# Optimization experiments

Hardware: AMD Instinct MI355X
Metric: run time of the kernel (lower is better)

The kernel has to match this reference:

```python
import jax, jax.numpy as jnp
import numpy as np

B, N, T, D = 2, 4, 512, 1024
DK, H, E = 64, 8, 6
D_ATTN = 512
DV = D_ATTN // H            # 64
DKP = 2 * DK                # PoPE doubles key dim -> 128
HE = H * E                  # 48
R = max(DK // 4, 1)         # LoRA rank 16
DA = int(DK * 1.618)        # 103
CC = D_ATTN                 # concat dim 512
DPG = max(int(CC * 0.618), 1)  # 316
ND = N * D
ROUTE_TEMP = 1.0


def _sinkhorn(M, n_iters=6):
    M = jnp.exp(M)
    for _ in range(n_iters):
        M = M / jnp.sum(M, -1, keepdims=True)
        M = M / jnp.sum(M, -2, keepdims=True)
    return M


def _pope(x, phi):
    mu = jax.nn.softplus(x)
    return jnp.concatenate([mu * jnp.cos(phi), mu * jnp.sin(phi)], -1)


def setup_inputs():
    ks = iter(jax.random.split(jax.random.key(0), 24))
    def rn(s, sc=0.01):
        return jax.random.normal(next(ks), s, jnp.float32) * sc
    return {
        'stream': jax.random.normal(next(ks), (B, N, T, D), jnp.float32),
        'freqs': 10000.0 ** (jnp.arange(DK, dtype=jnp.float32) / DK),
        'pope_delta_raw': jnp.zeros((DK,), jnp.float32),
        'W_q_w': rn((H, DK, D)), 'W_k_w': rn((H, DK, D)), 'W_v_w': rn((H, DV, D)),
        'q_router_w': rn((H, E, D), 0.02), 'kv_router_w': rn((H, E, D), 0.02),
        'lora_A_q': rn((HE, D, R)), 'lora_B_q': jnp.zeros((HE, R, DK), jnp.float32),
        'lora_A_k': rn((HE, D, R)), 'lora_B_k': jnp.zeros((HE, R, DK), jnp.float32),
        'lora_A_v': rn((HE, D, R)), 'lora_B_v': jnp.zeros((HE, R, DV), jnp.float32),
        'alpha_up_w': rn((HE, D, DA)), 'alpha_down_w': rn((HE, DA, DKP)),
        'beta_up_w': rn((HE, D, DA)), 'beta_down_w': rn((HE, DA, 1)),
        'mhc_norm_w': jnp.ones((HE, ND), jnp.float32),
        'phi_pre_w': rn((HE, N, ND)), 'phi_post_w': rn((HE, N, ND)),
        'phi_res_w': rn((HE, N * N, ND)),
        'b_pre': jnp.zeros((HE, N), jnp.float32), 'b_post': jnp.zeros((HE, N), jnp.float32),
        'b_res': jnp.zeros((HE, N, N), jnp.float32),
        'alpha_pre': jnp.ones((HE,), jnp.float32), 'alpha_post': jnp.ones((HE,), jnp.float32),
        'alpha_res': jnp.ones((HE,), jnp.float32),
        'batched_norm_w': jnp.ones((HE, D), jnp.float32),
        'W_pre_w': rn((HE, D, CC)), 'W_o_w': rn((D, CC)),
        'W_pg1_w': rn((HE, D, DPG)), 'W_pg2_w': rn((HE, DPG, D)),
    }


def reference(stream, freqs, pope_delta_raw, W_q_w, W_k_w, W_v_w, q_router_w, kv_router_w,
              lora_A_q, lora_B_q, lora_A_k, lora_B_k, lora_A_v, lora_B_v,
              alpha_up_w, alpha_down_w, beta_up_w, beta_down_w,
              mhc_norm_w, phi_pre_w, phi_post_w, phi_res_w, b_pre, b_post, b_res,
              alpha_pre, alpha_post, alpha_res, batched_norm_w,
              W_pre_w, W_o_w, W_pg1_w, W_pg2_w):
    positions = jnp.arange(T, dtype=jnp.float32)
    # ---- per-head top-1 routing (eval-mode argmax, straight-through probs) ----
    route_in = jnp.mean(stream, axis=1)                                # (B,T,D)
    q_logits = jnp.clip(jnp.einsum('btd,hed->hbte', route_in, q_router_w), -10, 10)
    kv_logits = jnp.clip(jnp.einsum('btd,hed->hbte', route_in, kv_router_w), -10, 10)
    q_probs = jax.nn.softmax(q_logits / ROUTE_TEMP, -1)
    kv_probs = jax.nn.softmax(kv_logits / ROUTE_TEMP, -1)
    q_oh = jax.nn.one_hot(jnp.argmax(q_logits, -1), E, dtype=stream.dtype)
    kv_oh = jax.nn.one_hot(jnp.argmax(kv_logits, -1), E, dtype=stream.dtype)
    eff_q = q_probs + jax.lax.stop_gradient(q_oh - q_probs)            # (H,B,T,E)
    eff_kv = kv_probs + jax.lax.stop_gradient(kv_oh - kv_probs)
    eff_q = eff_q.transpose(0, 3, 1, 2).reshape(HE, B, T)              # h-major, k=h*E+e
    eff_kv = eff_kv.transpose(0, 3, 1, 2).reshape(HE, B, T)
    # ---- batched MHC over all HE experts (dense form of active-set gather) ----
    x = stream.transpose(0, 2, 1, 3).reshape(B, T, ND)
    x = x * jax.lax.rsqrt(jnp.mean(jnp.square(x), -1, keepdims=True) + 1e-8)
    H_pre = jax.nn.sigmoid(alpha_pre[:, None, None, None] *
                           jnp.einsum('btd,knd->kbtn', x, phi_pre_w * mhc_norm_w[:, None, :])
                           + b_pre[:, None, None, :])
    H_post = 2 * jax.nn.sigmoid(alpha_post[:, None, None, None] *
                                jnp.einsum('btd,knd->kbtn', x, phi_post_w * mhc_norm_w[:, None, :])
                                + b_post[:, None, None, :])
    res = jnp.einsum('btd,knd->kbtn', x, phi_res_w * mhc_norm_w[:, None, :]).reshape(HE, B, T, N, N)
    H_res = _sinkhorn(alpha_res[:, None, None, None, None] * res + b_res[:, None, None, :, :])
    h_e = jnp.einsum('kbtn,bntd->kbtd', H_pre, stream)                 # (HE,B,T,D)
    h_e = h_e * jax.lax.rsqrt(jnp.mean(jnp.square(h_e), -1, keepdims=True) + 1e-8) * batched_norm_w[:, None, None, :]
    # ---- expert q/k/v with LoRA + PoPE ----
    phi = positions[:, None] * freqs[None, :]                          # (T,DK)
    phi_k = phi - 2 * jnp.pi * jax.nn.sigmoid(pope_delta_raw)[None, :]
    Wq = jnp.repeat(W_q_w, E, 0); Wk = jnp.repeat(W_k_w, E, 0); Wv = jnp.repeat(W_v_w, E, 0)
    def lora(h, A, Bm):
        return jnp.einsum('kbtr,kro->kbto', jax.nn.silu(jnp.einsum('kbtd,kdr->kbtr', h, A)), Bm)
    def l2n(v):
        return v * jax.lax.rsqrt(jnp.sum(jnp.square(v), -1, keepdims=True) + 1e-12)
    q_p = l2n(jnp.einsum('kbtd,kod->kbto', h_e, Wq) + lora(h_e, lora_A_q, lora_B_q))
    k_p = l2n(jnp.einsum('kbtd,kod->kbto', h_e, Wk) + lora(h_e, lora_A_k, lora_B_k))
    v_p = jnp.einsum('kbtd,kod->kbto', h_e, Wv) + lora(h_e, lora_A_v, lora_B_v)
    qmask = (jnp.arange(HE) % E > 0).astype(stream.dtype)[:, None, None, None]  # expert 0 = no-op for Q
    q_out = _pope(q_p, phi[None, None]) * qmask                        # (HE,B,T,DKP)
    k_out = _pope(k_p, phi_k[None, None])
    a_out = jax.nn.sigmoid(jnp.einsum('kbta,kap->kbtp', jax.nn.silu(jnp.einsum('kbtd,kda->kbta', h_e, alpha_up_w)), alpha_down_w))
    b_out = jax.nn.sigmoid(jnp.einsum('kbta,kap->kbtp', jax.nn.silu(jnp.einsum('kbtd,kda->kbta', h_e, beta_up_w)), beta_down_w))
    def mix(w, vals):
        return (w[..., None] * vals).reshape(H, E, B, T, vals.shape[-1]).sum(1)  # (H,B,T,*)
    q_buf = mix(eff_q, q_out); k_buf = mix(eff_kv, k_out); v_buf = mix(eff_kv, v_p)
    a_buf = mix(eff_kv, a_out); b_buf = mix(eff_kv, b_out)
    # ---- KDA delta-rule state recursion via lax.scan over time ----
    def step(S, xs):
        q_t, k_t, v_t, a_t, b_t = xs                                   # (H,B,dim)
        aS = a_t[..., None] * S                                        # (H,B,DKP,DV)
        ktaS = jnp.einsum('hbd,hbde->hbe', k_t, aS)
        S = aS + b_t[..., None] * (k_t[..., None] * (v_t - ktaS)[..., None, :])
        return S, jnp.einsum('hbd,hbde->hbe', q_t, S)
    tf = lambda z: jnp.moveaxis(z, 2, 0)                               # (T,H,B,*)
    S0 = jnp.zeros((H, B, DKP, DV), stream.dtype)
    _, outs = jax.lax.scan(step, S0, (tf(q_buf), tf(k_buf), tf(v_buf), tf(a_buf), tf(b_buf)))
    attn = outs.transpose(2, 0, 1, 3).reshape(B, T, H * DV)            # concat heads
    # ---- gates, output projection, MHC write-back ----
    pre_gate = jax.nn.sigmoid(jnp.einsum('kbt,kbtd,kdc->btc', eff_kv, h_e, W_pre_w))
    pg = jax.nn.silu(jnp.einsum('kbtd,kdp->kbtp', h_e, W_pg1_w))
    post_gate = jax.nn.sigmoid(jnp.einsum('kbt,kbtp,kpd->btd', eff_kv, pg, W_pg2_w))
    y = jnp.einsum('btc,dc->btd', attn * pre_gate, W_o_w) * post_gate
    Hres_acc = jnp.einsum('kbt,kbtnm->btnm', eff_kv, H_res) / H
    Hpost_acc = jnp.einsum('kbt,kbtn->btn', eff_kv, H_post) / H
    return jnp.einsum('btnm,bmtd->bntd', Hres_acc, stream) + jnp.einsum('btn,btd->bntd', Hpost_acc, y)
```

## Files before the change

### kernel.cpp

```cpp
#include <hip/hip_runtime.h>
#include <math.h>

#define DEV static __device__ __forceinline__

#define B_   2
#define N_   4
#define T_   512
#define D_   1024
#define DK_  64
#define H_   8
#define E_   6
#define DV_  64
#define DKP_ 128
#define HE_  48
#define R_   16
#define DA_  103
#define CC_  512
#define DPG_ 316
#define ND_  4096
#define U_   1024

typedef unsigned short u16;
typedef __attribute__((ext_vector_type(8))) unsigned short us8;
typedef __attribute__((ext_vector_type(8))) short bhalf8;
typedef __attribute__((ext_vector_type(4))) float f32x4;

struct P {
  const float *stream, *freqs, *pope_delta;
  const float *W_q, *W_k, *W_v, *q_rw, *kv_rw;
  const float *lA_q, *lB_q, *lA_k, *lB_k, *lA_v, *lB_v;
  const float *a_up, *a_dn, *b_up, *b_dn;
  const float *mhc_norm, *phi_pre, *phi_post, *phi_res;
  const float *b_pre, *b_post, *b_res, *al_pre, *al_post, *al_res;
  const float *bn_w, *W_pre, *W_o, *W_pg1, *W_pg2;
  int *qsel, *kvsel, *qcnt, *kvcnt, *qlist, *kvlist;
  float *scale, *mhc_partial;
  float *Hpre_q, *Hpre_kv, *Hres, *Hpost;
  float *kv_lin, *aup, *bup, *pre_logit, *post_logit;
  float *la_k, *la_v, *la_q, *q_lin;
  float *a_buf, *b_buf, *q_buf, *k_buf, *v_buf;
  float *attn, *y;
  float *out;
  u16 *he_kvB, *he_qB, *pgB;
  u16 *Bt0, *Bt1, *Bt2, *Bt3, *Bt4;
  float *phiT, *he_kvF, *he_qF, *pgF;
  float *WqT, *WkT, *WvT, *WoT;
};

DEV float sigm(float x){ return 1.f/(1.f+expf(-x)); }
DEV float softplus_(float x){ return x>0.f ? x+log1pf(expf(-x)) : log1pf(expf(x)); }
DEV float silu_(float x){ return x*sigm(x); }
DEV u16 f2b(float x){ unsigned u = __float_as_uint(x); u += 0x7FFFu + ((u>>16)&1u); return (u16)(u>>16); }

DEV float block_reduce_sum(float v, float* sm){
  __syncthreads();
  int lane = threadIdx.x & 63, w = threadIdx.x >> 6;
  for (int off=32; off; off>>=1) v += __shfl_down(v, off, 64);
  if (lane==0) sm[w] = v;
  __syncthreads();
  if (threadIdx.x == 0){
    float s = 0; int nw = blockDim.x >> 6;
    for (int i=0;i<nw;i++) s += sm[i];
    sm[0] = s;
  }
  __syncthreads();
  return sm[0];
}


__global__ void k_prep0(P p){
  int j = blockIdx.x; int k = j/24, r = j%24;
  const float* src;
  if (r < 4)      src = p.phi_pre  + (size_t)(k*4+r)*ND_;
  else if (r < 8) src = p.phi_post + (size_t)(k*4+(r-4))*ND_;
  else            src = p.phi_res  + (size_t)(k*16+(r-8))*ND_;
  const float* mn = p.mhc_norm + (size_t)k*ND_;
  u16* d = p.Bt0 + (size_t)j*ND_;
  for (int i = threadIdx.x; i < ND_; i += 256) d[i] = f2b(src[i]*mn[i]);
}

__global__ void k_prep1d(P p){
  int r = blockIdx.x, g = blockIdx.y, h = g/E_;
  u16* drow = p.Bt1 + (size_t)g*1216*1024 + (size_t)(r<128 ? r : 1194 + (r-128))*1024;
  const float* srow = (r<64) ? (p.W_k + ((size_t)h*64 + r)*1024)
                   : (r<128) ? (p.W_v + ((size_t)h*64 + (r-64))*1024) : nullptr;
  for (int k2 = threadIdx.x; k2 < 1024; k2 += 256)
    drow[k2] = (r<128) ? f2b(srow[k2]) : (u16)0;
}

__global__ void k_prep2d(P p){
  int r = blockIdx.x, g = blockIdx.y, h = g/E_;
  u16* drow = p.Bt2 + (size_t)g*128*1024 + (size_t)r*1024;
  const float* srow = p.W_q + ((size_t)h*64 + r)*1024;
  for (int k2 = threadIdx.x; k2 < 1024; k2 += 256) drow[k2] = f2b(srow[k2]);
}

__global__ void k_prep4(P p){
  int r = blockIdx.x;
  u16* drow = p.Bt4 + (size_t)r*512;
  const float* srow = p.W_o + (size_t)r*512;
  for (int c = threadIdx.x; c < 512; c += 256) drow[c] = f2b(srow[c]);
}

__global__ void k_prept(const float* src, long sstride, int ld, int ncols,
                        u16* dst, long dstride, int dld, int K, int Ksrc){
  __shared__ float t[32][33];
  const float* S = src + (size_t)blockIdx.z*sstride;
  u16* Dp = dst + (size_t)blockIdx.z*dstride;
  int k0 = blockIdx.x*32, c0 = blockIdx.y*32;
  int tx = threadIdx.x & 31, ty = threadIdx.x >> 5;
  #pragma unroll
  for (int i=0;i<32;i+=8){
    int k = k0+ty+i, c = c0+tx;
    t[ty+i][tx] = (k < Ksrc && c < ncols) ? S[(size_t)k*ld + c] : 0.f;
  }
  __syncthreads();
  #pragma unroll
  for (int i=0;i<32;i+=8){
    int c = c0+ty+i, k = k0+tx;
    if (c < ncols && k < K) Dp[(size_t)c*dld + k] = f2b(t[tx][ty+i]);
  }
}


__global__ void k_route(P p){
  int u = blockIdx.x, b = u>>9, t = u&511;
  __shared__ float ri[D_];
  __shared__ float lg[2][HE_];
  int tid = threadIdx.x;
  for (int d = tid; d < D_; d += 256){
    float s = 0;
    #pragma unroll
    for (int n = 0; n < N_; n++) s += p.stream[(((size_t)(b*N_+n)*T_)+t)*D_ + d];
    ri[d] = s * 0.25f;
  }
  __syncthreads();
  int lane = tid & 63, wv = tid >> 6;
  for (int j = wv; j < 2*HE_; j += 4){
    const float* w = (j < HE_ ? p.q_rw : p.kv_rw) + (size_t)(j % HE_)*D_;
    float acc = 0;
    for (int d = lane; d < D_; d += 64) acc += ri[d]*w[d];
    for (int off=32; off; off>>=1) acc += __shfl_down(acc, off, 64);
    if (lane==0) lg[j/HE_][j%HE_] = acc;
  }
  __syncthreads();
  if (tid < 16){
    int h = tid & 7, which = tid >> 3;
    const float* L = lg[which] + h*E_;
    float best = fminf(fmaxf(L[0],-10.f),10.f); int bi=0;
    for (int e=1;e<E_;e++){ float v=fminf(fmaxf(L[e],-10.f),10.f); if (v>best){best=v;bi=e;} }
    int g = h*E_+bi;
    if (which==0){ p.qsel[h*U_+u]=bi;  int pos=atomicAdd(&p.qcnt[g],1);  p.qlist[g*U_+pos]=u; }
    else         { p.kvsel[h*U_+u]=bi; int pos=atomicAdd(&p.kvcnt[g],1); p.kvlist[g*U_+pos]=u; }
  }
}

__global__ void k_xscale(P p){
  int u = blockIdx.x, b = u>>9, t = u&511;
  __shared__ float sm[8];
  float ss = 0;
  for (int i = threadIdx.x; i < ND_; i += 256){
    int n = i >> 10, d = i & 1023;
    float v = p.stream[(((size_t)(b*N_+n)*T_)+t)*D_ + d];
    ss += v*v;
  }
  ss = block_reduce_sum(ss, sm);
  if (threadIdx.x==0) p.scale[u] = rsqrtf(ss/(float)ND_ + 1e-8f);
}


template<int MODE>
__global__ __launch_bounds__(256) void k_mgemm(P p){
  const int n0 = blockIdx.x * 128;
  const int m0 = blockIdx.y * 128;
  const int g  = blockIdx.z;
  const int h  = g / E_;
  int K, NO, cnt;
  const int* list = nullptr;
  const u16* Bsrc;
  if (MODE==0){ K=1024; NO=1152; cnt=U_; Bsrc=p.Bt0; }
  else if (MODE==1){ K=1024; NO=1194; cnt=p.kvcnt[g]; list=p.kvlist+g*U_; Bsrc=p.Bt1+(size_t)g*1216*1024; }
  else if (MODE==2){ K=1024; NO=80;   cnt=p.qcnt[g];  list=p.qlist +g*U_; Bsrc=p.Bt2+(size_t)g*128*1024; }
  else if (MODE==3){ K=320;  NO=1024; cnt=p.kvcnt[g]; list=p.kvlist+g*U_; Bsrc=p.Bt3+(size_t)g*1024*320; }
  else { K=512; NO=1024; cnt=U_; Bsrc=p.Bt4; }
  if (m0 >= cnt) return;
  const int rows = min(128, cnt - m0);

  __shared__ u16 Asl[128*32];
  __shared__ u16 Bsl[128*32];
  __shared__ int toks[128];
  const int tid = threadIdx.x;
  if (tid < 128){
    if (MODE==0||MODE==4) toks[tid] = m0 + tid;
    else toks[tid] = (tid < rows) ? list[m0+tid] : list[m0];
  }
  __syncthreads();

  f32x4 acc[4][4];
  #pragma unroll
  for (int i=0;i<4;i++)
    #pragma unroll
    for (int j=0;j<4;j++) acc[i][j] = (f32x4)(0.f);

  const int lane = tid & 63, wv = tid >> 6;
  const int wr = (wv>>1)*64, wc = (wv&1)*64;
  const int l16 = lane & 15, kce = lane >> 4;

  for (int k0 = 0; k0 < K; k0 += 32){
    #pragma unroll
    for (int pass=0; pass<2; pass++){
      int m = (tid>>2) + pass*64;
      int kc4 = tid & 3;
      int ks = k0 + kc4*8;
      us8 av;
      if (MODE==1){
        int u = toks[m];
        av = *(const us8*)&p.he_kvB[((size_t)(h*U_+u))*1024 + ks];
      } else if (MODE==2){
        int u = toks[m];
        av = *(const us8*)&p.he_qB[((size_t)(h*U_+u))*1024 + ks];
      } else if (MODE==3){
        int u = toks[m];
        av = *(const us8*)&p.pgB[((size_t)(h*U_+u))*320 + ks];
      } else if (MODE==0){
        int u = toks[m]; int bb=u>>9, tt=u&511;
        int fk = g*1024 + ks;
        int n = fk>>10, d = fk&1023;
        const float* sp = p.stream + (((size_t)(bb*N_+n)*T_)+tt)*D_ + d;
        float sc = p.scale[u];
        float4 x0 = *(const float4*)sp, x1 = *(const float4*)(sp+4);
        av[0]=f2b(x0.x*sc); av[1]=f2b(x0.y*sc); av[2]=f2b(x0.z*sc); av[3]=f2b(x0.w*sc);
        av[4]=f2b(x1.x*sc); av[5]=f2b(x1.y*sc); av[6]=f2b(x1.z*sc); av[7]=f2b(x1.w*sc);
      } else {
        int u = toks[m];
        const float* ap = p.attn + (size_t)u*CC_ + ks;
        const float* pp = p.pre_logit + (size_t)u*CC_ + ks;
        float4 a0 = *(const float4*)ap, a1 = *(const float4*)(ap+4);
        float4 q0 = *(const float4*)pp, q1 = *(const float4*)(pp+4);
        av[0]=f2b(a0.x*sigm(q0.x)); av[1]=f2b(a0.y*sigm(q0.y));
        av[2]=f2b(a0.z*sigm(q0.z)); av[3]=f2b(a0.w*sigm(q0.w));
        av[4]=f2b(a1.x*sigm(q1.x)); av[5]=f2b(a1.y*sigm(q1.y));
        av[6]=f2b(a1.z*sigm(q1.z)); av[7]=f2b(a1.w*sigm(q1.w));
      }
      *(us8*)&Asl[m*32 + kc4*8] = av;
    }
    #pragma unroll
    for (int pass=0; pass<2; pass++){
      int n = (tid>>2) + pass*64;
      int kc4 = tid & 3;
      int ks = k0 + kc4*8;
      int gn = n0 + n;
      us8 bv = (us8)((u16)0);
      if (MODE==1){ if (gn < 1216) bv = *(const us8*)&Bsrc[(size_t)gn*1024 + ks]; }
      else if (MODE==0){ bv = *(const us8*)&Bsrc[(size_t)gn*4096 + g*1024 + ks]; }
      else if (MODE==2){ bv = *(const us8*)&Bsrc[(size_t)gn*1024 + ks]; }
      else if (MODE==3){ bv = *(const us8*)&Bsrc[(size_t)gn*320 + ks]; }
      else { bv = *(const us8*)&Bsrc[(size_t)gn*512 + ks]; }
      *(us8*)&Bsl[n*32 + kc4*8] = bv;
    }
    __syncthreads();
    bhalf8 af[4], bf4[4];
    #pragma unroll
    for (int i=0;i<4;i++) af[i] = *(const bhalf8*)&Asl[(wr + i*16 + l16)*32 + kce*8];
    #pragma unroll
    for (int j=0;j<4;j++) bf4[j] = *(const bhalf8*)&Bsl[(wc + j*16 + l16)*32 + kce*8];
    #pragma unroll
    for (int i=0;i<4;i++)
      #pragma unroll
      for (int j=0;j<4;j++)
        acc[i][j] = __builtin_amdgcn_mfma_f32_16x16x32_bf16(af[i], bf4[j], acc[i][j], 0, 0, 0);
    __syncthreads();
  }

  #pragma unroll
  for (int i=0;i<4;i++){
    #pragma unroll
    for (int r=0;r<4;r++){
      int rl = wr + i*16 + kce*4 + r;
      if (rl >= rows) continue;
      int u = toks[rl];
      #pragma unroll
      for (int j=0;j<4;j++){
        int cg = n0 + wc + j*16 + l16;
        if (cg >= NO) continue;
        float v = acc[i][j][r];
        if (MODE==0){
          p.mhc_partial[(size_t)g*U_*1152 + (size_t)u*1152 + cg] = v;
        } else if (MODE==1){
          size_t base = (size_t)(h*U_+u);
          if (cg < 128)       p.kv_lin[base*128 + cg] = v;
          else if (cg < 231)  p.aup[base*DA_ + (cg-128)] = silu_(v);
          else if (cg < 334)  p.bup[base*DA_ + (cg-231)] = silu_(v);
          else if (cg < 846)  atomicAdd(&p.pre_logit[(size_t)u*CC_ + (cg-334)], v);
          else if (cg < 1162) p.pgB[base*320 + (cg-846)] = f2b(silu_(v));
          else if (cg < 1178) p.la_k[base*R_ + (cg-1162)] = silu_(v);
          else                p.la_v[base*R_ + (cg-1178)] = silu_(v);
        } else if (MODE==2){
          size_t base = (size_t)(h*U_+u);
          if (cg < 64) p.q_lin[base*64 + cg] = v;
          else         p.la_q[base*R_ + (cg-64)] = silu_(v);
        } else if (MODE==3){
          atomicAdd(&p.post_logit[(size_t)u*D_ + cg], v);
        } else {
          p.y[(size_t)u*D_ + cg] = v * sigm(p.post_logit[(size_t)u*D_ + cg]);
        }
      }
    }
  }
}

#define BM 128
#define BN 128
#define BKF 32

template<int MODE>
__global__ __launch_bounds__(256) void k_gemm_f32(P p){
  const int n0 = blockIdx.x * BN;
  const int m0 = blockIdx.y * BM;
  const int g  = blockIdx.z;
  const int h  = g / E_;
  int K, NO, cnt, kbase = 0;
  const int* list = nullptr;
  if (MODE==0){ K=1024; NO=1152; cnt=U_; kbase = g*1024; }
  else if (MODE==1){ K=D_;   NO=1194; cnt=p.kvcnt[g]; list=p.kvlist + g*U_; }
  else if (MODE==2){ K=D_;   NO=80;   cnt=p.qcnt[g];  list=p.qlist  + g*U_; }
  else if (MODE==3){ K=DPG_; NO=D_;   cnt=p.kvcnt[g]; list=p.kvlist + g*U_; }
  else { K=CC_; NO=D_; cnt=U_; }
  if (m0 >= cnt) return;
  const int rows = min(BM, cnt - m0);

  __shared__ __align__(16) float As[BKF][BM+4];
  __shared__ __align__(16) float Bs[BKF][BN+4];
  __shared__ int toks[BM];
  const int tid = threadIdx.x;
  for (int i = tid; i < BM; i += 256){
    if (MODE==1||MODE==2||MODE==3) toks[i] = (i < rows) ? list[m0+i] : 0;
    else toks[i] = m0 + i;
  }
  __syncthreads();

  float acc[8][8];
  #pragma unroll
  for (int i=0;i<8;i++)
    #pragma unroll
    for(int j=0;j<8;j++) acc[i][j]=0.f;
  const int wave = tid >> 6, lane = tid & 63;
  const int wr = wave >> 1, wc = wave & 1;
  const int lr = lane >> 3, lc = lane & 7;
  const int a0 = wr*64 + lr*8, b0 = wc*64 + lc*8;

  for (int k0 = 0; k0 < K; k0 += BKF){
    #pragma unroll
    for (int i=0;i<16;i++){
      int idx = tid + 256*i;
      int r = idx >> 5, kk = idx & 31;
      int kg = k0 + kk;
      float v = 0.f;
      if (r < rows && kg < K){
        int u = toks[r];
        if (MODE==0){
          int kgg = kbase + kg;
          int b=u>>9, t=u&511, n=kgg>>10, d=kgg&1023;
          v = p.stream[(((size_t)(b*N_+n)*T_)+t)*D_ + d] * p.scale[u];
        } else if (MODE==1) v = p.he_kvF[((size_t)(h*U_+u))*D_ + kg];
        else if (MODE==2)   v = p.he_qF [((size_t)(h*U_+u))*D_ + kg];
        else if (MODE==3)   v = p.pgF  [((size_t)(h*U_+u))*DPG_ + kg];
        else {
          size_t o = (size_t)u*CC_ + kg;
          v = p.attn[o] * sigm(p.pre_logit[o]);
        }
      }
      As[kk][r] = v;
    }
    #pragma unroll
    for (int i=0;i<16;i++){
      int idx = tid + 256*i;
      int kk = idx >> 7, c = idx & 127;
      int kg = k0 + kk, cg = n0 + c;
      float v = 0.f;
      if (kg < K && cg < NO){
        if (MODE==0) v = p.phiT[(size_t)(kbase+kg)*1152 + cg];
        else if (MODE==1){
          const float* ptr; int ld, loc;
          if (cg < 64){        ptr = p.WkT   + (size_t)h*D_*64;   ld=64;   loc=cg; }
          else if (cg < 128){  ptr = p.WvT   + (size_t)h*D_*64;   ld=64;   loc=cg-64; }
          else if (cg < 231){  ptr = p.a_up  + (size_t)g*D_*DA_;  ld=DA_;  loc=cg-128; }
          else if (cg < 334){  ptr = p.b_up  + (size_t)g*D_*DA_;  ld=DA_;  loc=cg-231; }
          else if (cg < 846){  ptr = p.W_pre + (size_t)g*D_*CC_;  ld=CC_;  loc=cg-334; }
          else if (cg < 1162){ ptr = p.W_pg1 + (size_t)g*D_*DPG_; ld=DPG_; loc=cg-846; }
          else if (cg < 1178){ ptr = p.lA_k  + (size_t)g*D_*R_;   ld=R_;   loc=cg-1162; }
          else {               ptr = p.lA_v  + (size_t)g*D_*R_;   ld=R_;   loc=cg-1178; }
          v = ptr[(size_t)kg*ld + loc];
        }
        else if (MODE==2){
          if (cg < 64) v = p.WqT[(size_t)h*D_*64 + (size_t)kg*64 + cg];
          else v = p.lA_q[(size_t)g*D_*R_ + (size_t)kg*R_ + (cg-64)];
        }
        else if (MODE==3) v = p.W_pg2[(size_t)g*DPG_*D_ + (size_t)kg*D_ + cg];
        else v = p.WoT[(size_t)kg*D_ + cg];
      }
      Bs[kk][c] = v;
    }
    __syncthreads();
    #pragma unroll 8
    for (int kk=0; kk<BKF; kk++){
      float a[8], b[8];
      *(float4*)&a[0] = *(const float4*)&As[kk][a0];
      *(float4*)&a[4] = *(const float4*)&As[kk][a0+4];
      *(float4*)&b[0] = *(const float4*)&Bs[kk][b0];
      *(float4*)&b[4] = *(const float4*)&Bs[kk][b0+4];
      #pragma unroll
      for (int i=0;i<8;i++)
        #pragma unroll
        for (int j=0;j<8;j++) acc[i][j] += a[i]*b[j];
    }
    __syncthreads();
  }

  #pragma unroll
  for (int i=0;i<8;i++){
    int rl = a0 + i;
    if (rl >= rows) continue;
    int u = toks[rl];
    #pragma unroll
    for (int j=0;j<8;j++){
      int cg = n0 + b0 + j;
      if (cg >= NO) continue;
      float v = acc[i][j];
      if (MODE==0){
        p.mhc_partial[(size_t)g*U_*1152 + (size_t)u*1152 + cg] = v;
      } else if (MODE==1){
        size_t base = (size_t)(h*U_+u);
        if (cg < 128)       p.kv_lin[base*128 + cg] = v;
        else if (cg < 231)  p.aup[base*DA_ + (cg-128)] = silu_(v);
        else if (cg < 334)  p.bup[base*DA_ + (cg-231)] = silu_(v);
        else if (cg < 846)  atomicAdd(&p.pre_logit[(size_t)u*CC_ + (cg-334)], v);
        else if (cg < 1162) p.pgF[base*DPG_ + (cg-846)] = silu_(v);
        else if (cg < 1178) p.la_k[base*R_ + (cg-1162)] = silu_(v);
        else                p.la_v[base*R_ + (cg-1178)] = silu_(v);
      } else if (MODE==2){
        size_t base = (size_t)(h*U_+u);
        if (cg < 64) p.q_lin[base*64 + cg] = v;
        else         p.la_q[base*R_ + (cg-64)] = silu_(v);
      } else if (MODE==3){
        atomicAdd(&p.post_logit[(size_t)u*D_ + cg], v);
      } else {
        p.y[(size_t)u*D_ + cg] = v * sigm(p.post_logit[(size_t)u*D_ + cg]);
      }
    }
  }
}

__global__ void k_tr(const float* src, float* dst, int R, int C){
  __shared__ float t[32][33];
  int m = blockIdx.z;
  const float* S = src + (size_t)m*R*C;
  float* Dp = dst + (size_t)m*R*C;
  int c0 = blockIdx.x*32, r0 = blockIdx.y*32;
  int tx = threadIdx.x & 31, ty = threadIdx.x >> 5;
  #pragma unroll
  for (int i=0;i<32;i+=8)
    t[ty+i][tx] = S[(size_t)(r0+ty+i)*C + c0+tx];
  __syncthreads();
  #pragma unroll
  for (int i=0;i<32;i+=8)
    Dp[(size_t)(c0+ty+i)*R + r0+tx] = t[tx][ty+i];
}

__global__ void k_phiT(P p){
  __shared__ float t[64][65];
  int jt = blockIdx.x % 18, dt = blockIdx.x / 18;
  int tx = threadIdx.x & 63, ty = threadIdx.x >> 6;
  #pragma unroll
  for (int i=0;i<64;i+=4){
    int j = jt*64 + ty + i;
    int k = j/24, r = j%24;
    const float* src;
    if (r < 4)      src = p.phi_pre  + (size_t)(k*4+r)*ND_;
    else if (r < 8) src = p.phi_post + (size_t)(k*4+(r-4))*ND_;
    else            src = p.phi_res  + (size_t)(k*16+(r-8))*ND_;
    int d = dt*64 + tx;
    t[ty+i][tx] = src[d] * p.mhc_norm[(size_t)k*ND_ + d];
  }
  __syncthreads();
  #pragma unroll
  for (int i=0;i<64;i+=4){
    int d = dt*64 + ty + i;
    p.phiT[(size_t)d*1152 + jt*64 + tx] = t[tx][ty+i];
  }
}


DEV float lgread(const float* Pp, int j){
  const size_t S = (size_t)U_*1152;
  return Pp[j] + Pp[j+S] + Pp[j+2*S] + Pp[j+3*S];
}

__global__ void k_mhcsel(P p){
  int u = blockIdx.x;
  int tid = threadIdx.x;
  __shared__ float racc[8][16];
  __shared__ float pacc[8][4];
  if (tid < 8){
    int h = tid;
    const float* lg = p.mhc_partial + (size_t)u*1152;
    int kq = h*E_ + p.qsel[h*U_+u];
    for (int n=0;n<4;n++)
      p.Hpre_q[(size_t)(h*U_+u)*4 + n] = sigm(p.al_pre[kq]*lgread(lg,kq*24+n) + p.b_pre[kq*4+n]);
    int kk = h*E_ + p.kvsel[h*U_+u];
    for (int n=0;n<4;n++)
      p.Hpre_kv[(size_t)(h*U_+u)*4 + n] = sigm(p.al_pre[kk]*lgread(lg,kk*24+n) + p.b_pre[kk*4+n]);
    for (int n=0;n<4;n++)
      pacc[h][n] = 2.f*sigm(p.al_post[kk]*lgread(lg,kk*24+4+n) + p.b_post[kk*4+n]);
    float M[4][4];
    for (int n=0;n<4;n++)
      for (int m=0;m<4;m++)
        M[n][m] = expf(p.al_res[kk]*lgread(lg,kk*24+8+n*4+m) + p.b_res[kk*16+n*4+m]);
    for (int it=0; it<6; it++){
      for (int n=0;n<4;n++){ float s=M[n][0]+M[n][1]+M[n][2]+M[n][3]; float r=1.f/s;
        for(int m=0;m<4;m++) M[n][m]*=r; }
      for (int m=0;m<4;m++){ float s=M[0][m]+M[1][m]+M[2][m]+M[3][m]; float r=1.f/s;
        for(int n=0;n<4;n++) M[n][m]*=r; }
    }
    for (int n=0;n<4;n++) for (int m=0;m<4;m++) racc[h][n*4+m] = M[n][m];
  }
  __syncthreads();
  if (tid < 16){
    float s=0; for (int h=0;h<8;h++) s += racc[h][tid];
    p.Hres[(size_t)u*16 + tid] = s * 0.125f;
  }
  if (tid < 4){
    float s=0; for (int h=0;h<8;h++) s += pacc[h][tid];
    p.Hpost[(size_t)u*4 + tid] = s * 0.125f;
  }
}

template<int BF>
__global__ void k_he(P p){
  int id = blockIdx.x;
  int path = id >> 13;
  int h = (id >> 10) & 7;
  int u = id & 1023;
  int b = u>>9, t = u&511;
  int sel = path ? p.kvsel[h*U_+u] : p.qsel[h*U_+u];
  int k = h*E_ + sel;
  const float* Hp = (path ? p.Hpre_kv : p.Hpre_q) + (size_t)(h*U_+u)*4;
  float w0=Hp[0], w1=Hp[1], w2=Hp[2], w3=Hp[3];
  float v[4];
  float ss = 0;
  int tid = threadIdx.x;
  #pragma unroll
  for (int j=0;j<4;j++){
    int d = tid + j*256;
    float s0 = p.stream[(((size_t)(b*N_+0)*T_)+t)*D_ + d];
    float s1 = p.stream[(((size_t)(b*N_+1)*T_)+t)*D_ + d];
    float s2 = p.stream[(((size_t)(b*N_+2)*T_)+t)*D_ + d];
    float s3 = p.stream[(((size_t)(b*N_+3)*T_)+t)*D_ + d];
    v[j] = w0*s0 + w1*s1 + w2*s2 + w3*s3;
    ss += v[j]*v[j];
  }
  __shared__ float sm[8];
  ss = block_reduce_sum(ss, sm);
  float sc = rsqrtf(ss/(float)D_ + 1e-8f);
  #pragma unroll
  for (int j=0;j<4;j++){
    int d = tid + j*256;
    float o = v[j]*sc*p.bn_w[(size_t)k*D_ + d];
    if (BF){
      u16* out = (path ? p.he_kvB : p.he_qB) + (size_t)(h*U_+u)*D_;
      out[d] = f2b(o);
    } else {
      float* out = (path ? p.he_kvF : p.he_qF) + (size_t)(h*U_+u)*D_;
      out[d] = o;
    }
  }
}

__global__ void k_stage2(P p){
  int id = blockIdx.x;
  int h = id >> 10, u = id & 1023;
  int t = u & 511;
  int k = h*E_ + p.kvsel[h*U_+u];
  size_t base = (size_t)(h*U_+u);
  __shared__ float s_au[DA_], s_bu[DA_], s_lk[R_], s_lv[R_], s_kl[64], s_vl[64];
  int tid = threadIdx.x;
  if (tid < DA_){ s_au[tid] = p.aup[base*DA_+tid]; s_bu[tid] = p.bup[base*DA_+tid]; }
  if (tid < R_){ s_lk[tid] = p.la_k[base*R_+tid]; s_lv[tid] = p.la_v[base*R_+tid]; }
  if (tid >= 64 && tid < 128){
    s_kl[tid-64] = p.kv_lin[base*128 + (tid-64)];
    s_vl[tid-64] = p.kv_lin[base*128 + 64 + (tid-64)];
  }
  __syncthreads();
  {
    float acc = 0;
    const float* W = p.a_dn + (size_t)k*DA_*DKP_;
    for (int a=0;a<DA_;a++) acc += s_au[a]*W[a*DKP_ + tid];
    p.a_buf[base*DKP_ + tid] = sigm(acc);
  }
  if (tid == 0){
    float acc = 0;
    const float* W = p.b_dn + (size_t)k*DA_;
    for (int a=0;a<DA_;a++) acc += s_bu[a]*W[a];
    p.b_buf[base] = sigm(acc);
  }
  if (tid < 64){
    int o = tid;
    float lbk=0.f, lbv=0.f;
    for (int r=0;r<R_;r++){
      lbk += s_lk[r]*p.lB_k[((size_t)k*R_+r)*DK_ + o];
      lbv += s_lv[r]*p.lB_v[((size_t)k*R_+r)*DV_ + o];
    }
    float kl = s_kl[o] + lbk;
    float ss = kl*kl;
    for (int off=1; off<64; off<<=1) ss += __shfl_xor(ss, off, 64);
    float kp = kl * rsqrtf(ss + 1e-12f);
    float mu = softplus_(kp);
    float ph = (float)t * p.freqs[o] - 6.2831855f * sigm(p.pope_delta[o]);
    p.k_buf[base*DKP_ + o]      = mu * cosf(ph);
    p.k_buf[base*DKP_ + 64 + o] = mu * sinf(ph);
    p.v_buf[base*DV_ + o] = s_vl[o] + lbv;
  }
}

__global__ void k_stage2q(P p){
  int id = blockIdx.x;
  int h = id >> 10, u = id & 1023;
  int t = u & 511;
  int sel = p.qsel[h*U_+u];
  size_t base = (size_t)(h*U_+u);
  int o = threadIdx.x;
  if (sel == 0){
    p.q_buf[base*DKP_ + o] = 0.f;
    p.q_buf[base*DKP_ + 64 + o] = 0.f;
    return;
  }
  int k = h*E_ + sel;
  float lbq = 0.f;
  for (int r=0;r<R_;r++) lbq += p.la_q[base*R_+r]*p.lB_q[((size_t)k*R_+r)*DK_+o];
  float ql = p.q_lin[base*64 + o] + lbq;
  float ss = ql*ql;
  for (int off=1; off<64; off<<=1) ss += __shfl_xor(ss, off, 64);
  float qp = ql*rsqrtf(ss + 1e-12f);
  float mu = softplus_(qp);
  float ph = (float)t * p.freqs[o];
  p.q_buf[base*DKP_ + o]      = mu*cosf(ph);
  p.q_buf[base*DKP_ + 64 + o] = mu*sinf(ph);
}

__global__ __launch_bounds__(512) void k_scan(P p){
  int h = blockIdx.x >> 1, b = blockIdx.x & 1;
  int tid = threadIdx.x;
  int e = tid & 63, d8 = tid >> 6;
  float S[16];
  #pragma unroll
  for (int i=0;i<16;i++) S[i]=0.f;
  __shared__ float sq[128], sk[128], sa[128], sv[64];
  __shared__ float sb[1];
  __shared__ float part[8][64];
  __shared__ float part2[8][64];
  float r0=0.f, r1=0.f;
  {
    size_t base = (size_t)(h*U_ + b*T_);
    if (tid < 128){ r0 = p.q_buf[base*128+tid]; r1 = p.k_buf[base*128+tid]; }
    else if (tid < 256){ r0 = p.a_buf[base*128 + (tid-128)]; }
    else if (tid < 320){ r0 = p.v_buf[base*64 + (tid-256)]; }
    else if (tid == 320){ r0 = p.b_buf[base]; }
  }
  for (int t=0;t<T_;t++){
    if (tid < 128){ sq[tid]=r0; sk[tid]=r1; }
    else if (tid < 256){ sa[tid-128]=r0; }
    else if (tid < 320){ sv[tid-256]=r0; }
    else if (tid == 320){ sb[0]=r0; }
    __syncthreads();
    if (t+1 < T_){
      size_t base = (size_t)(h*U_ + b*T_ + t+1);
      if (tid < 128){ r0 = p.q_buf[base*128+tid]; r1 = p.k_buf[base*128+tid]; }
      else if (tid < 256){ r0 = p.a_buf[base*128 + (tid-128)]; }
      else if (tid < 320){ r0 = p.v_buf[base*64 + (tid-256)]; }
      else if (tid == 320){ r0 = p.b_buf[base]; }
    }
    int db = d8*16;
    float pa = 0.f;
    #pragma unroll
    for (int i=0;i<16;i++) pa += sk[db+i]*sa[db+i]*S[i];
    part[d8][e] = pa;
    __syncthreads();
    float w = sv[e];
    #pragma unroll
    for (int j=0;j<8;j++) w -= part[j][e];
    float bs = sb[0];
    float o = 0.f;
    #pragma unroll
    for (int i=0;i<16;i++){
      S[i] = sa[db+i]*S[i] + bs*sk[db+i]*w;
      o += sq[db+i]*S[i];
    }
    part2[d8][e] = o;
    __syncthreads();
    if (tid < 64){
      float s=0;
      #pragma unroll
      for (int j=0;j<8;j++) s += part2[j][tid];
      p.attn[(size_t)(b*T_+t)*CC_ + h*64 + tid] = s;
    }
  }
}

__global__ void k_final(P p){
  int u = blockIdx.x, b=u>>9, t=u&511;
  __shared__ float hr[16], hp[4];
  if (threadIdx.x < 16) hr[threadIdx.x] = p.Hres[(size_t)u*16+threadIdx.x];
  if (threadIdx.x < 4)  hp[threadIdx.x] = p.Hpost[(size_t)u*4+threadIdx.x];
  __syncthreads();
  for (int d = threadIdx.x; d < D_; d += 256){
    float yv = p.y[(size_t)u*D_ + d];
    float sm0 = p.stream[(((size_t)(b*N_+0)*T_)+t)*D_ + d];
    float sm1 = p.stream[(((size_t)(b*N_+1)*T_)+t)*D_ + d];
    float sm2 = p.stream[(((size_t)(b*N_+2)*T_)+t)*D_ + d];
    float sm3 = p.stream[(((size_t)(b*N_+3)*T_)+t)*D_ + d];
    #pragma unroll
    for (int n=0;n<4;n++){
      float v = hr[n*4+0]*sm0 + hr[n*4+1]*sm1 + hr[n*4+2]*sm2 + hr[n*4+3]*sm3 + hp[n]*yv;
      p.out[(((size_t)(b*N_+n)*T_)+t)*D_ + d] = v;
    }
  }
}


extern "C" void kernel_launch(void* const* d_in, const int* in_sizes, int n_in,
                              void* d_out, int out_size, void* d_ws, size_t ws_size,
                              hipStream_t stream){
  P p;
  p.stream = (const float*)d_in[0];
  p.freqs = (const float*)d_in[1];
  p.pope_delta = (const float*)d_in[2];
  p.W_q = (const float*)d_in[3]; p.W_k = (const float*)d_in[4]; p.W_v = (const float*)d_in[5];
  p.q_rw = (const float*)d_in[6]; p.kv_rw = (const float*)d_in[7];
  p.lA_q = (const float*)d_in[8];  p.lB_q = (const float*)d_in[9];
  p.lA_k = (const float*)d_in[10]; p.lB_k = (const float*)d_in[11];
  p.lA_v = (const float*)d_in[12]; p.lB_v = (const float*)d_in[13];
  p.a_up = (const float*)d_in[14]; p.a_dn = (const float*)d_in[15];
  p.b_up = (const float*)d_in[16]; p.b_dn = (const float*)d_in[17];
  p.mhc_norm = (const float*)d_in[18];
  p.phi_pre = (const float*)d_in[19]; p.phi_post = (const float*)d_in[20]; p.phi_res = (const float*)d_in[21];
  p.b_pre = (const float*)d_in[22]; p.b_post = (const float*)d_in[23]; p.b_res = (const float*)d_in[24];
  p.al_pre = (const float*)d_in[25]; p.al_post = (const float*)d_in[26]; p.al_res = (const float*)d_in[27];
  p.bn_w = (const float*)d_in[28];
  p.W_pre = (const float*)d_in[29]; p.W_o = (const float*)d_in[30];
  p.W_pg1 = (const float*)d_in[31]; p.W_pg2 = (const float*)d_in[32];
  p.out = (float*)d_out;

  char* w = (char*)d_ws;
  size_t off = 0;
  auto alloc = [&](size_t bytes)->void*{
    void* r = w + off;
    off = (off + bytes + 255) & ~(size_t)255;
    return r;
  };
  p.qsel   = (int*)alloc(H_*U_*4);
  p.kvsel  = (int*)alloc(H_*U_*4);
  p.qcnt   = (int*)alloc(HE_*4);
  p.kvcnt  = (int*)alloc(HE_*4);
  p.qlist  = (int*)alloc((size_t)HE_*U_*4);
  p.kvlist = (int*)alloc((size_t)HE_*U_*4);
  p.scale  = (float*)alloc(U_*4);
  p.mhc_partial = (float*)alloc((size_t)4*U_*1152*4);
  p.Hpre_q  = (float*)alloc((size_t)H_*U_*4*4);
  p.Hpre_kv = (float*)alloc((size_t)H_*U_*4*4);
  p.Hres    = (float*)alloc((size_t)U_*16*4);
  p.Hpost   = (float*)alloc((size_t)U_*4*4);
  p.kv_lin  = (float*)alloc((size_t)H_*U_*128*4);
  p.aup     = (float*)alloc((size_t)H_*U_*DA_*4);
  p.bup     = (float*)alloc((size_t)H_*U_*DA_*4);
  p.pre_logit  = (float*)alloc((size_t)U_*CC_*4);
  p.post_logit = (float*)alloc((size_t)U_*D_*4);
  p.la_k    = (float*)alloc((size_t)H_*U_*R_*4);
  p.la_v    = (float*)alloc((size_t)H_*U_*R_*4);
  p.la_q    = (float*)alloc((size_t)H_*U_*R_*4);
  p.q_lin   = (float*)alloc((size_t)H_*U_*64*4);
  p.a_buf   = (float*)alloc((size_t)H_*U_*DKP_*4);
  p.b_buf   = (float*)alloc((size_t)H_*U_*4);
  p.q_buf   = (float*)alloc((size_t)H_*U_*DKP_*4);
  p.k_buf   = (float*)alloc((size_t)H_*U_*DKP_*4);
  p.v_buf   = (float*)alloc((size_t)H_*U_*DV_*4);
  p.attn    = (float*)alloc((size_t)U_*CC_*4);
  p.y       = (float*)alloc((size_t)U_*D_*4);
  size_t common_off = off;

  p.he_kvB = (u16*)alloc((size_t)H_*U_*D_*2);
  p.he_qB  = (u16*)alloc((size_t)H_*U_*D_*2);
  p.pgB    = (u16*)alloc((size_t)H_*U_*320*2);
  p.Bt0    = (u16*)alloc((size_t)1152*4096*2);
  p.Bt1    = (u16*)alloc((size_t)HE_*1216*1024*2);
  p.Bt2    = (u16*)alloc((size_t)HE_*128*1024*2);
  p.Bt3    = (u16*)alloc((size_t)HE_*1024*320*2);
  p.Bt4    = (u16*)alloc((size_t)1024*512*2);
  bool mfma = (off <= ws_size);

  if (!mfma){
    off = common_off;
    p.phiT   = (float*)alloc((size_t)ND_*1152*4);
    p.he_kvF = (float*)alloc((size_t)H_*U_*D_*4);
    p.he_qF  = (float*)alloc((size_t)H_*U_*D_*4);
    p.pgF    = (float*)alloc((size_t)H_*U_*DPG_*4);
    p.WqT    = (float*)alloc((size_t)H_*D_*64*4);
    p.WkT    = (float*)alloc((size_t)H_*D_*64*4);
    p.WvT    = (float*)alloc((size_t)H_*D_*64*4);
    p.WoT    = (float*)alloc((size_t)CC_*D_*4);
    if (off > ws_size) return;
  }

  hipMemsetAsync(p.qcnt, 0, HE_*4, stream);
  hipMemsetAsync(p.kvcnt, 0, HE_*4, stream);
  hipMemsetAsync(p.pre_logit, 0, (size_t)U_*CC_*4, stream);
  hipMemsetAsync(p.post_logit, 0, (size_t)U_*D_*4, stream);

  if (mfma){
    hipMemsetAsync(p.pgB, 0, (size_t)H_*U_*320*2, stream);
    hipMemsetAsync(p.Bt2, 0, (size_t)HE_*128*1024*2, stream);
    k_prep0<<<1152,256,0,stream>>>(p);
    k_prep1d<<<dim3(150,48),256,0,stream>>>(p);
    size_t b1s = (size_t)1216*1024;
    k_prept<<<dim3(32, 4,48),256,0,stream>>>(p.a_up,  (long)1024*DA_, DA_, DA_, p.Bt1+ 128*1024, b1s, 1024, 1024, 1024);
    k_prept<<<dim3(32, 4,48),256,0,stream>>>(p.b_up,  (long)1024*DA_, DA_, DA_, p.Bt1+ 231*1024, b1s, 1024, 1024, 1024);
    k_prept<<<dim3(32,16,48),256,0,stream>>>(p.W_pre, (long)1024*CC_, CC_, CC_, p.Bt1+ 334*1024, b1s, 1024, 1024, 1024);
    k_prept<<<dim3(32,10,48),256,0,stream>>>(p.W_pg1, (long)1024*DPG_,DPG_,DPG_,p.Bt1+ 846*1024, b1s, 1024, 1024, 1024);
    k_prept<<<dim3(32, 1,48),256,0,stream>>>(p.lA_k,  (long)1024*R_,  R_,  R_,  p.Bt1+1162*1024, b1s, 1024, 1024, 1024);
    k_prept<<<dim3(32, 1,48),256,0,stream>>>(p.lA_v,  (long)1024*R_,  R_,  R_,  p.Bt1+1178*1024, b1s, 1024, 1024, 1024);
    k_prep2d<<<dim3(64,48),256,0,stream>>>(p);
    k_prept<<<dim3(32, 1,48),256,0,stream>>>(p.lA_q,  (long)1024*R_,  R_,  R_,  p.Bt2+  64*1024, (long)128*1024, 1024, 1024, 1024);
    k_prept<<<dim3(10,32,48),256,0,stream>>>(p.W_pg2, (long)DPG_*1024,1024,1024,p.Bt3,           (long)1024*320,  320,  320,  316);
    k_prep4<<<1024,256,0,stream>>>(p);

    k_route<<<U_,256,0,stream>>>(p);
    k_xscale<<<U_,256,0,stream>>>(p);
    k_mgemm<0><<<dim3(9,8,4),256,0,stream>>>(p);
    k_mhcsel<<<U_,64,0,stream>>>(p);
    k_he<1><<<2*H_*U_,256,0,stream>>>(p);
    k_mgemm<1><<<dim3(10,8,48),256,0,stream>>>(p);
    k_mgemm<2><<<dim3(1,8,48),256,0,stream>>>(p);
    k_stage2<<<H_*U_,128,0,stream>>>(p);
    k_stage2q<<<H_*U_,64,0,stream>>>(p);
    k_mgemm<3><<<dim3(8,8,48),256,0,stream>>>(p);
    k_scan<<<16,512,0,stream>>>(p);
    k_mgemm<4><<<dim3(8,8,1),256,0,stream>>>(p);
    k_final<<<U_,256,0,stream>>>(p);
  } else {
    k_tr<<<dim3(32,2,8),256,0,stream>>>(p.W_q, p.WqT, 64, 1024);
    k_tr<<<dim3(32,2,8),256,0,stream>>>(p.W_k, p.WkT, 64, 1024);
    k_tr<<<dim3(32,2,8),256,0,stream>>>(p.W_v, p.WvT, 64, 1024);
    k_tr<<<dim3(16,32,1),256,0,stream>>>(p.W_o, p.WoT, 1024, 512);
    k_phiT<<<1152,256,0,stream>>>(p);
    k_route<<<U_,256,0,stream>>>(p);
    k_xscale<<<U_,256,0,stream>>>(p);
    k_gemm_f32<0><<<dim3(9,8,4),256,0,stream>>>(p);
    k_mhcsel<<<U_,64,0,stream>>>(p);
    k_he<0><<<2*H_*U_,256,0,stream>>>(p);
    k_gemm_f32<1><<<dim3(10,8,48),256,0,stream>>>(p);
    k_gemm_f32<2><<<dim3(1,8,48),256,0,stream>>>(p);
    k_stage2<<<H_*U_,128,0,stream>>>(p);
    k_stage2q<<<H_*U_,64,0,stream>>>(p);
    k_gemm_f32<3><<<dim3(8,8,48),256,0,stream>>>(p);
    k_scan<<<16,512,0,stream>>>(p);
    k_gemm_f32<4><<<dim3(8,8,1),256,0,stream>>>(p);
    k_final<<<U_,256,0,stream>>>(p);
  }
}
```

Baseline: 1.537 ms.

## Fuse xscale into routing, merge stage2q into stage2, restructure scan, drop fp32 fallback

The RMS scale computation moves into the routing kernel, which also writes a pre-scaled bf16 copy of the stream. The first MFMA GEMM then loads bf16 directly instead of converting fp32 on the fly. The q-side stage2 work is folded into the kv stage2 kernel, so one launch replaces two. The sequential scan is rewritten with 256 threads holding 32 state elements each, reading k/a from global memory into registers and double-buffering q in shared memory, which cuts barriers per step. The unused fp32 fallback path is removed, and the fallback no longer exists if the workspace is too small.

```diff
diff --git a/kernel.cpp b/kernel.cpp
--- a/kernel.cpp
+++ b/kernel.cpp
@@ -41,10 +41,9 @@
   float *a_buf, *b_buf, *q_buf, *k_buf, *v_buf;
   float *attn, *y;
   float *out;
+  u16 *xb;
   u16 *he_kvB, *he_qB, *pgB;
   u16 *Bt0, *Bt1, *Bt2, *Bt3, *Bt4;
-  float *phiT, *he_kvF, *he_qF, *pgF;
-  float *WqT, *WkT, *WvT, *WoT;
 };
 
 DEV float sigm(float x){ return 1.f/(1.f+expf(-x)); }
@@ -127,14 +126,30 @@
   int u = blockIdx.x, b = u>>9, t = u&511;
   __shared__ float ri[D_];
   __shared__ float lg[2][HE_];
+  __shared__ float sm[8];
   int tid = threadIdx.x;
-  for (int d = tid; d < D_; d += 256){
-    float s = 0;
-    #pragma unroll
-    for (int n = 0; n < N_; n++) s += p.stream[(((size_t)(b*N_+n)*T_)+t)*D_ + d];
-    ri[d] = s * 0.25f;
-  }
-  __syncthreads();
+  float sv[4][4]; float ss = 0.f;
+  #pragma unroll
+  for (int j=0;j<4;j++){
+    int d = tid + j*256;
+    float acc = 0;
+    #pragma unroll
+    for (int n = 0; n < 4; n++){
+      float v = p.stream[(((size_t)(b*N_+n)*T_)+t)*D_ + d];
+      sv[j][n] = v; acc += v; ss += v*v;
+    }
+    ri[d] = acc * 0.25f;
+  }
+  ss = block_reduce_sum(ss, sm);
+  float sc = rsqrtf(ss/(float)ND_ + 1e-8f);
+  if (tid==0) p.scale[u] = sc;
+  #pragma unroll
+  for (int j=0;j<4;j++){
+    int d = tid + j*256;
+    #pragma unroll
+    for (int n=0;n<4;n++)
+      p.xb[(size_t)u*ND_ + n*D_ + d] = f2b(sv[j][n]*sc);
+  }
   int lane = tid & 63, wv = tid >> 6;
   for (int j = wv; j < 2*HE_; j += 4){
     const float* w = (j < HE_ ? p.q_rw : p.kv_rw) + (size_t)(j % HE_)*D_;
@@ -153,19 +168,6 @@
     if (which==0){ p.qsel[h*U_+u]=bi;  int pos=atomicAdd(&p.qcnt[g],1);  p.qlist[g*U_+pos]=u; }
     else         { p.kvsel[h*U_+u]=bi; int pos=atomicAdd(&p.kvcnt[g],1); p.kvlist[g*U_+pos]=u; }
   }
-}
-
-__global__ void k_xscale(P p){
-  int u = blockIdx.x, b = u>>9, t = u&511;
-  __shared__ float sm[8];
-  float ss = 0;
-  for (int i = threadIdx.x; i < ND_; i += 256){
-    int n = i >> 10, d = i & 1023;
-    float v = p.stream[(((size_t)(b*N_+n)*T_)+t)*D_ + d];
-    ss += v*v;
-  }
-  ss = block_reduce_sum(ss, sm);
-  if (threadIdx.x==0) p.scale[u] = rsqrtf(ss/(float)ND_ + 1e-8f);
 }
 
 
@@ -223,14 +225,8 @@
         int u = toks[m];
         av = *(const us8*)&p.pgB[((size_t)(h*U_+u))*320 + ks];
       } else if (MODE==0){
-        int u = toks[m]; int bb=u>>9, tt=u&511;
-        int fk = g*1024 + ks;
-        int n = fk>>10, d = fk&1023;
-        const float* sp = p.stream + (((size_t)(bb*N_+n)*T_)+tt)*D_ + d;
-        float sc = p.scale[u];
-        float4 x0 = *(const float4*)sp, x1 = *(const float4*)(sp+4);
-        av[0]=f2b(x0.x*sc); av[1]=f2b(x0.y*sc); av[2]=f2b(x0.z*sc); av[3]=f2b(x0.w*sc);
-        av[4]=f2b(x1.x*sc); av[5]=f2b(x1.y*sc); av[6]=f2b(x1.z*sc); av[7]=f2b(x1.w*sc);
+        int u = toks[m];
+        av = *(const us8*)&p.xb[(size_t)u*ND_ + g*1024 + ks];
       } else {
         int u = toks[m];
         const float* ap = p.attn + (size_t)u*CC_ + ks;
@@ -309,187 +305,6 @@
   }
 }
 
-#define BM 128
-#define BN 128
-#define BKF 32
-
-template<int MODE>
-__global__ __launch_bounds__(256) void k_gemm_f32(P p){
-  const int n0 = blockIdx.x * BN;
-  const int m0 = blockIdx.y * BM;
-  const int g  = blockIdx.z;
-  const int h  = g / E_;
-  int K, NO, cnt, kbase = 0;
-  const int* list = nullptr;
-  if (MODE==0){ K=1024; NO=1152; cnt=U_; kbase = g*1024; }
-  else if (MODE==1){ K=D_;   NO=1194; cnt=p.kvcnt[g]; list=p.kvlist + g*U_; }
-  else if (MODE==2){ K=D_;   NO=80;   cnt=p.qcnt[g];  list=p.qlist  + g*U_; }
-  else if (MODE==3){ K=DPG_; NO=D_;   cnt=p.kvcnt[g]; list=p.kvlist + g*U_; }
-  else { K=CC_; NO=D_; cnt=U_; }
-  if (m0 >= cnt) return;
-  const int rows = min(BM, cnt - m0);
-
-  __shared__ __align__(16) float As[BKF][BM+4];
-  __shared__ __align__(16) float Bs[BKF][BN+4];
-  __shared__ int toks[BM];
-  const int tid = threadIdx.x;
-  for (int i = tid; i < BM; i += 256){
-    if (MODE==1||MODE==2||MODE==3) toks[i] = (i < rows) ? list[m0+i] : 0;
-    else toks[i] = m0 + i;
-  }
-  __syncthreads();
-
-  float acc[8][8];
-  #pragma unroll
-  for (int i=0;i<8;i++)
-    #pragma unroll
-    for(int j=0;j<8;j++) acc[i][j]=0.f;
-  const int wave = tid >> 6, lane = tid & 63;
-  const int wr = wave >> 1, wc = wave & 1;
-  const int lr = lane >> 3, lc = lane & 7;
-  const int a0 = wr*64 + lr*8, b0 = wc*64 + lc*8;
-
-  for (int k0 = 0; k0 < K; k0 += BKF){
-    #pragma unroll
-    for (int i=0;i<16;i++){
-      int idx = tid + 256*i;
-      int r = idx >> 5, kk = idx & 31;
-      int kg = k0 + kk;
-      float v = 0.f;
-      if (r < rows && kg < K){
-        int u = toks[r];
-        if (MODE==0){
-          int kgg = kbase + kg;
-          int b=u>>9, t=u&511, n=kgg>>10, d=kgg&1023;
-          v = p.stream[(((size_t)(b*N_+n)*T_)+t)*D_ + d] * p.scale[u];
-        } else if (MODE==1) v = p.he_kvF[((size_t)(h*U_+u))*D_ + kg];
-        else if (MODE==2)   v = p.he_qF [((size_t)(h*U_+u))*D_ + kg];
-        else if (MODE==3)   v = p.pgF  [((size_t)(h*U_+u))*DPG_ + kg];
-        else {
-          size_t o = (size_t)u*CC_ + kg;
-          v = p.attn[o] * sigm(p.pre_logit[o]);
-        }
-      }
-      As[kk][r] = v;
-    }
-    #pragma unroll
-    for (int i=0;i<16;i++){
-      int idx = tid + 256*i;
-      int kk = idx >> 7, c = idx & 127;
-      int kg = k0 + kk, cg = n0 + c;
-      float v = 0.f;
-      if (kg < K && cg < NO){
-        if (MODE==0) v = p.phiT[(size_t)(kbase+kg)*1152 + cg];
-        else if (MODE==1){
-          const float* ptr; int ld, loc;
-          if (cg < 64){        ptr = p.WkT   + (size_t)h*D_*64;   ld=64;   loc=cg; }
-          else if (cg < 128){  ptr = p.WvT   + (size_t)h*D_*64;   ld=64;   loc=cg-64; }
-          else if (cg < 231){  ptr = p.a_up  + (size_t)g*D_*DA_;  ld=DA_;  loc=cg-128; }
-          else if (cg < 334){  ptr = p.b_up  + (size_t)g*D_*DA_;  ld=DA_;  loc=cg-231; }
-          else if (cg < 846){  ptr = p.W_pre + (size_t)g*D_*CC_;  ld=CC_;  loc=cg-334; }
-          else if (cg < 1162){ ptr = p.W_pg1 + (size_t)g*D_*DPG_; ld=DPG_; loc=cg-846; }
-          else if (cg < 1178){ ptr = p.lA_k  + (size_t)g*D_*R_;   ld=R_;   loc=cg-1162; }
-          else {               ptr = p.lA_v  + (size_t)g*D_*R_;   ld=R_;   loc=cg-1178; }
-          v = ptr[(size_t)kg*ld + loc];
-        }
-        else if (MODE==2){
-          if (cg < 64) v = p.WqT[(size_t)h*D_*64 + (size_t)kg*64 + cg];
-          else v = p.lA_q[(size_t)g*D_*R_ + (size_t)kg*R_ + (cg-64)];
-        }
-        else if (MODE==3) v = p.W_pg2[(size_t)g*DPG_*D_ + (size_t)kg*D_ + cg];
-        else v = p.WoT[(size_t)kg*D_ + cg];
-      }
-      Bs[kk][c] = v;
-    }
-    __syncthreads();
-    #pragma unroll 8
-    for (int kk=0; kk<BKF; kk++){
-      float a[8], b[8];
-      *(float4*)&a[0] = *(const float4*)&As[kk][a0];
-      *(float4*)&a[4] = *(const float4*)&As[kk][a0+4];
-      *(float4*)&b[0] = *(const float4*)&Bs[kk][b0];
-      *(float4*)&b[4] = *(const float4*)&Bs[kk][b0+4];
-      #pragma unroll
-      for (int i=0;i<8;i++)
-        #pragma unroll
-        for (int j=0;j<8;j++) acc[i][j] += a[i]*b[j];
-    }
-    __syncthreads();
-  }
-
-  #pragma unroll
-  for (int i=0;i<8;i++){
-    int rl = a0 + i;
-    if (rl >= rows) continue;
-    int u = toks[rl];
-    #pragma unroll
-    for (int j=0;j<8;j++){
-      int cg = n0 + b0 + j;
-      if (cg >= NO) continue;
-      float v = acc[i][j];
-      if (MODE==0){
-        p.mhc_partial[(size_t)g*U_*1152 + (size_t)u*1152 + cg] = v;
-      } else if (MODE==1){
-        size_t base = (size_t)(h*U_+u);
-        if (cg < 128)       p.kv_lin[base*128 + cg] = v;
-        else if (cg < 231)  p.aup[base*DA_ + (cg-128)] = silu_(v);
-        else if (cg < 334)  p.bup[base*DA_ + (cg-231)] = silu_(v);
-        else if (cg < 846)  atomicAdd(&p.pre_logit[(size_t)u*CC_ + (cg-334)], v);
-        else if (cg < 1162) p.pgF[base*DPG_ + (cg-846)] = silu_(v);
-        else if (cg < 1178) p.la_k[base*R_ + (cg-1162)] = silu_(v);
-        else                p.la_v[base*R_ + (cg-1178)] = silu_(v);
-      } else if (MODE==2){
-        size_t base = (size_t)(h*U_+u);
-        if (cg < 64) p.q_lin[base*64 + cg] = v;
-        else         p.la_q[base*R_ + (cg-64)] = silu_(v);
-      } else if (MODE==3){
-        atomicAdd(&p.post_logit[(size_t)u*D_ + cg], v);
-      } else {
-        p.y[(size_t)u*D_ + cg] = v * sigm(p.post_logit[(size_t)u*D_ + cg]);
-      }
-    }
-  }
-}
-
-__global__ void k_tr(const float* src, float* dst, int R, int C){
-  __shared__ float t[32][33];
-  int m = blockIdx.z;
-  const float* S = src + (size_t)m*R*C;
-  float* Dp = dst + (size_t)m*R*C;
-  int c0 = blockIdx.x*32, r0 = blockIdx.y*32;
-  int tx = threadIdx.x & 31, ty = threadIdx.x >> 5;
-  #pragma unroll
-  for (int i=0;i<32;i+=8)
-    t[ty+i][tx] = S[(size_t)(r0+ty+i)*C + c0+tx];
-  __syncthreads();
-  #pragma unroll
-  for (int i=0;i<32;i+=8)
-    Dp[(size_t)(c0+ty+i)*R + r0+tx] = t[tx][ty+i];
-}
-
-__global__ void k_phiT(P p){
-  __shared__ float t[64][65];
-  int jt = blockIdx.x % 18, dt = blockIdx.x / 18;
-  int tx = threadIdx.x & 63, ty = threadIdx.x >> 6;
-  #pragma unroll
-  for (int i=0;i<64;i+=4){
-    int j = jt*64 + ty + i;
-    int k = j/24, r = j%24;
-    const float* src;
-    if (r < 4)      src = p.phi_pre  + (size_t)(k*4+r)*ND_;
-    else if (r < 8) src = p.phi_post + (size_t)(k*4+(r-4))*ND_;
-    else            src = p.phi_res  + (size_t)(k*16+(r-8))*ND_;
-    int d = dt*64 + tx;
-    t[ty+i][tx] = src[d] * p.mhc_norm[(size_t)k*ND_ + d];
-  }
-  __syncthreads();
-  #pragma unroll
-  for (int i=0;i<64;i+=4){
-    int d = dt*64 + ty + i;
-    p.phiT[(size_t)d*1152 + jt*64 + tx] = t[tx][ty+i];
-  }
-}
-
 
 DEV float lgread(const float* Pp, int j){
   const size_t S = (size_t)U_*1152;
@@ -535,7 +350,6 @@
   }
 }
 
-template<int BF>
 __global__ void k_he(P p){
   int id = blockIdx.x;
   int path = id >> 13;
@@ -562,17 +376,11 @@
   __shared__ float sm[8];
   ss = block_reduce_sum(ss, sm);
   float sc = rsqrtf(ss/(float)D_ + 1e-8f);
+  u16* out = (path ? p.he_kvB : p.he_qB) + (size_t)(h*U_+u)*D_;
   #pragma unroll
   for (int j=0;j<4;j++){
     int d = tid + j*256;
-    float o = v[j]*sc*p.bn_w[(size_t)k*D_ + d];
-    if (BF){
-      u16* out = (path ? p.he_kvB : p.he_qB) + (size_t)(h*U_+u)*D_;
-      out[d] = f2b(o);
-    } else {
-      float* out = (path ? p.he_kvF : p.he_qF) + (size_t)(h*U_+u)*D_;
-      out[d] = o;
-    }
+    out[d] = f2b(v[j]*sc*p.bn_w[(size_t)k*D_ + d]);
   }
 }
 
@@ -580,26 +388,27 @@
   int id = blockIdx.x;
   int h = id >> 10, u = id & 1023;
   int t = u & 511;
-  int k = h*E_ + p.kvsel[h*U_+u];
+  int kkv = h*E_ + p.kvsel[h*U_+u];
   size_t base = (size_t)(h*U_+u);
-  __shared__ float s_au[DA_], s_bu[DA_], s_lk[R_], s_lv[R_], s_kl[64], s_vl[64];
+  __shared__ float s_au[DA_], s_bu[DA_], s_lk[R_], s_lv[R_], s_lq[R_], s_kl[64], s_vl[64], s_ql[64];
   int tid = threadIdx.x;
   if (tid < DA_){ s_au[tid] = p.aup[base*DA_+tid]; s_bu[tid] = p.bup[base*DA_+tid]; }
-  if (tid < R_){ s_lk[tid] = p.la_k[base*R_+tid]; s_lv[tid] = p.la_v[base*R_+tid]; }
+  if (tid < R_){ s_lk[tid] = p.la_k[base*R_+tid]; s_lv[tid] = p.la_v[base*R_+tid]; s_lq[tid] = p.la_q[base*R_+tid]; }
   if (tid >= 64 && tid < 128){
     s_kl[tid-64] = p.kv_lin[base*128 + (tid-64)];
     s_vl[tid-64] = p.kv_lin[base*128 + 64 + (tid-64)];
   }
+  if (tid < 64) s_ql[tid] = p.q_lin[base*64 + tid];
   __syncthreads();
   {
     float acc = 0;
-    const float* W = p.a_dn + (size_t)k*DA_*DKP_;
+    const float* W = p.a_dn + (size_t)kkv*DA_*DKP_;
     for (int a=0;a<DA_;a++) acc += s_au[a]*W[a*DKP_ + tid];
     p.a_buf[base*DKP_ + tid] = sigm(acc);
   }
   if (tid == 0){
     float acc = 0;
-    const float* W = p.b_dn + (size_t)k*DA_;
+    const float* W = p.b_dn + (size_t)kkv*DA_;
     for (int a=0;a<DA_;a++) acc += s_bu[a]*W[a];
     p.b_buf[base] = sigm(acc);
   }
@@ -607,8 +416,8 @@
     int o = tid;
     float lbk=0.f, lbv=0.f;
     for (int r=0;r<R_;r++){
-      lbk += s_lk[r]*p.lB_k[((size_t)k*R_+r)*DK_ + o];
-      lbv += s_lv[r]*p.lB_v[((size_t)k*R_+r)*DV_ + o];
+      lbk += s_lk[r]*p.lB_k[((size_t)kkv*R_+r)*DK_ + o];
+      lbv += s_lv[r]*p.lB_v[((size_t)kkv*R_+r)*DV_ + o];
     }
     float kl = s_kl[o] + lbk;
     float ss = kl*kl;
@@ -619,90 +428,76 @@
     p.k_buf[base*DKP_ + o]      = mu * cosf(ph);
     p.k_buf[base*DKP_ + 64 + o] = mu * sinf(ph);
     p.v_buf[base*DV_ + o] = s_vl[o] + lbv;
-  }
-}
-
-__global__ void k_stage2q(P p){
-  int id = blockIdx.x;
-  int h = id >> 10, u = id & 1023;
-  int t = u & 511;
-  int sel = p.qsel[h*U_+u];
-  size_t base = (size_t)(h*U_+u);
-  int o = threadIdx.x;
-  if (sel == 0){
-    p.q_buf[base*DKP_ + o] = 0.f;
-    p.q_buf[base*DKP_ + 64 + o] = 0.f;
-    return;
-  }
-  int k = h*E_ + sel;
-  float lbq = 0.f;
-  for (int r=0;r<R_;r++) lbq += p.la_q[base*R_+r]*p.lB_q[((size_t)k*R_+r)*DK_+o];
-  float ql = p.q_lin[base*64 + o] + lbq;
-  float ss = ql*ql;
-  for (int off=1; off<64; off<<=1) ss += __shfl_xor(ss, off, 64);
-  float qp = ql*rsqrtf(ss + 1e-12f);
-  float mu = softplus_(qp);
-  float ph = (float)t * p.freqs[o];
-  p.q_buf[base*DKP_ + o]      = mu*cosf(ph);
-  p.q_buf[base*DKP_ + 64 + o] = mu*sinf(ph);
-}
-
-__global__ __launch_bounds__(512) void k_scan(P p){
-  int h = blockIdx.x >> 1, b = blockIdx.x & 1;
-  int tid = threadIdx.x;
-  int e = tid & 63, d8 = tid >> 6;
-  float S[16];
-  #pragma unroll
-  for (int i=0;i<16;i++) S[i]=0.f;
-  __shared__ float sq[128], sk[128], sa[128], sv[64];
-  __shared__ float sb[1];
-  __shared__ float part[8][64];
-  __shared__ float part2[8][64];
-  float r0=0.f, r1=0.f;
-  {
-    size_t base = (size_t)(h*U_ + b*T_);
-    if (tid < 128){ r0 = p.q_buf[base*128+tid]; r1 = p.k_buf[base*128+tid]; }
-    else if (tid < 256){ r0 = p.a_buf[base*128 + (tid-128)]; }
-    else if (tid < 320){ r0 = p.v_buf[base*64 + (tid-256)]; }
-    else if (tid == 320){ r0 = p.b_buf[base]; }
-  }
+  } else {
+    int o = tid - 64;
+    int sel = p.qsel[h*U_+u];
+    if (sel == 0){
+      p.q_buf[base*DKP_ + o] = 0.f;
+      p.q_buf[base*DKP_ + 64 + o] = 0.f;
+    } else {
+      int kq = h*E_ + sel;
+      float lbq = 0.f;
+      for (int r=0;r<R_;r++) lbq += s_lq[r]*p.lB_q[((size_t)kq*R_+r)*DK_+o];
+      float ql = s_ql[o] + lbq;
+      float ss = ql*ql;
+      for (int off=1; off<64; off<<=1) ss += __shfl_xor(ss, off, 64);
+      float qp = ql*rsqrtf(ss + 1e-12f);
+      float mu = softplus_(qp);
+      float ph = (float)t * p.freqs[o];
+      p.q_buf[base*DKP_ + o]      = mu*cosf(ph);
+      p.q_buf[base*DKP_ + 64 + o] = mu*sinf(ph);
+    }
+  }
+}
+
+__global__ __launch_bounds__(256) void k_scan(P p){
+  const int h = blockIdx.x >> 1, b = blockIdx.x & 1;
+  const int tid = threadIdx.x;
+  const int e = tid & 63;
+  const int qd = __builtin_amdgcn_readfirstlane(tid >> 6);
+  const int d0 = qd * 32;
+  const size_t hb = (size_t)(h*U_ + b*T_);
+  float s[32];
+  #pragma unroll
+  for (int i=0;i<32;i++) s[i]=0.f;
+  __shared__ float sq[2][128];
+  __shared__ float part[2][4][64];
+  __shared__ float part2[4][64];
+  float rq = (tid<128) ? p.q_buf[hb*128 + tid] : 0.f;
+  if (tid<128) sq[0][tid] = rq;
+  rq = (tid<128) ? p.q_buf[(hb+1)*128 + tid] : 0.f;
+  __syncthreads();
   for (int t=0;t<T_;t++){
-    if (tid < 128){ sq[tid]=r0; sk[tid]=r1; }
-    else if (tid < 256){ sa[tid-128]=r0; }
-    else if (tid < 320){ sv[tid-256]=r0; }
-    else if (tid == 320){ sb[0]=r0; }
+    const int bb = t&1;
+    const size_t base = hb + t;
+    const float* kp = p.k_buf + base*128 + d0;
+    const float* ap = p.a_buf + base*128 + d0;
+    float kr[32], ar[32];
+    #pragma unroll
+    for (int i=0;i<32;i++){ kr[i]=kp[i]; ar[i]=ap[i]; }
+    float bs = p.b_buf[base];
+    float vv = p.v_buf[base*64 + e];
+    float pa = 0.f;
+    #pragma unroll
+    for (int i=0;i<32;i++) pa += (ar[i]*s[i])*kr[i];
+    part[bb][qd][e] = pa;
     __syncthreads();
-    if (t+1 < T_){
-      size_t base = (size_t)(h*U_ + b*T_ + t+1);
-      if (tid < 128){ r0 = p.q_buf[base*128+tid]; r1 = p.k_buf[base*128+tid]; }
-      else if (tid < 256){ r0 = p.a_buf[base*128 + (tid-128)]; }
-      else if (tid < 320){ r0 = p.v_buf[base*64 + (tid-256)]; }
-      else if (tid == 320){ r0 = p.b_buf[base]; }
-    }
-    int db = d8*16;
-    float pa = 0.f;
-    #pragma unroll
-    for (int i=0;i<16;i++) pa += sk[db+i]*sa[db+i]*S[i];
-    part[d8][e] = pa;
-    __syncthreads();
-    float w = sv[e];
-    #pragma unroll
-    for (int j=0;j<8;j++) w -= part[j][e];
-    float bs = sb[0];
+    float w = vv - (part[bb][0][e]+part[bb][1][e]+part[bb][2][e]+part[bb][3][e]);
+    float bw = bs * w;
     float o = 0.f;
     #pragma unroll
-    for (int i=0;i<16;i++){
-      S[i] = sa[db+i]*S[i] + bs*sk[db+i]*w;
-      o += sq[db+i]*S[i];
-    }
-    part2[d8][e] = o;
+    for (int i=0;i<32;i++){
+      s[i] = ar[i]*s[i] + bw*kr[i];
+      o += sq[bb][d0+i] * s[i];
+    }
+    if (tid < 128) sq[bb^1][tid] = rq;
+    part2[qd][e] = o;
     __syncthreads();
     if (tid < 64){
-      float s=0;
-      #pragma unroll
-      for (int j=0;j<8;j++) s += part2[j][tid];
-      p.attn[(size_t)(b*T_+t)*CC_ + h*64 + tid] = s;
-    }
+      float r = part2[0][tid]+part2[1][tid]+part2[2][tid]+part2[3][tid];
+      p.attn[(size_t)(b*T_+t)*CC_ + h*64 + tid] = r;
+    }
+    if (tid < 128 && t+2 < T_) rq = p.q_buf[(hb+t+2)*128 + tid];
   }
 }
 
@@ -785,8 +580,7 @@
   p.v_buf   = (float*)alloc((size_t)H_*U_*DV_*4);
   p.attn    = (float*)alloc((size_t)U_*CC_*4);
   p.y       = (float*)alloc((size_t)U_*D_*4);
-  size_t common_off = off;
-
+  p.xb      = (u16*)alloc((size_t)U_*ND_*2);
   p.he_kvB = (u16*)alloc((size_t)H_*U_*D_*2);
   p.he_qB  = (u16*)alloc((size_t)H_*U_*D_*2);
   p.pgB    = (u16*)alloc((size_t)H_*U_*320*2);
@@ -795,74 +589,38 @@
   p.Bt2    = (u16*)alloc((size_t)HE_*128*1024*2);
   p.Bt3    = (u16*)alloc((size_t)HE_*1024*320*2);
   p.Bt4    = (u16*)alloc((size_t)1024*512*2);
-  bool mfma = (off <= ws_size);
-
-  if (!mfma){
-    off = common_off;
-    p.phiT   = (float*)alloc((size_t)ND_*1152*4);
-    p.he_kvF = (float*)alloc((size_t)H_*U_*D_*4);
-    p.he_qF  = (float*)alloc((size_t)H_*U_*D_*4);
-    p.pgF    = (float*)alloc((size_t)H_*U_*DPG_*4);
-    p.WqT    = (float*)alloc((size_t)H_*D_*64*4);
-    p.WkT    = (float*)alloc((size_t)H_*D_*64*4);
-    p.WvT    = (float*)alloc((size_t)H_*D_*64*4);
-    p.WoT    = (float*)alloc((size_t)CC_*D_*4);
-    if (off > ws_size) return;
-  }
+  if (off > ws_size) return;
 
   hipMemsetAsync(p.qcnt, 0, HE_*4, stream);
   hipMemsetAsync(p.kvcnt, 0, HE_*4, stream);
   hipMemsetAsync(p.pre_logit, 0, (size_t)U_*CC_*4, stream);
   hipMemsetAsync(p.post_logit, 0, (size_t)U_*D_*4, stream);
-
-  if (mfma){
-    hipMemsetAsync(p.pgB, 0, (size_t)H_*U_*320*2, stream);
-    hipMemsetAsync(p.Bt2, 0, (size_t)HE_*128*1024*2, stream);
-    k_prep0<<<1152,256,0,stream>>>(p);
-    k_prep1d<<<dim3(150,48),256,0,stream>>>(p);
-    size_t b1s = (size_t)1216*1024;
-    k_prept<<<dim3(32, 4,48),256,0,stream>>>(p.a_up,  (long)1024*DA_, DA_, DA_, p.Bt1+ 128*1024, b1s, 1024, 1024, 1024);
-    k_prept<<<dim3(32, 4,48),256,0,stream>>>(p.b_up,  (long)1024*DA_, DA_, DA_, p.Bt1+ 231*1024, b1s, 1024, 1024, 1024);
-    k_prept<<<dim3(32,16,48),256,0,stream>>>(p.W_pre, (long)1024*CC_, CC_, CC_, p.Bt1+ 334*1024, b1s, 1024, 1024, 1024);
-    k_prept<<<dim3(32,10,48),256,0,stream>>>(p.W_pg1, (long)1024*DPG_,DPG_,DPG_,p.Bt1+ 846*1024, b1s, 1024, 1024, 1024);
-    k_prept<<<dim3(32, 1,48),256,0,stream>>>(p.lA_k,  (long)1024*R_,  R_,  R_,  p.Bt1+1162*1024, b1s, 1024, 1024, 1024);
-    k_prept<<<dim3(32, 1,48),256,0,stream>>>(p.lA_v,  (long)1024*R_,  R_,  R_,  p.Bt1+1178*1024, b1s, 1024, 1024, 1024);
-    k_prep2d<<<dim3(64,48),256,0,stream>>>(p);
-    k_prept<<<dim3(32, 1,48),256,0,stream>>>(p.lA_q,  (long)1024*R_,  R_,  R_,  p.Bt2+  64*1024, (long)128*1024, 1024, 1024, 1024);
-    k_prept<<<dim3(10,32,48),256,0,stream>>>(p.W_pg2, (long)DPG_*1024,1024,1024,p.Bt3,           (long)1024*320,  320,  320,  316);
-    k_prep4<<<1024,256,0,stream>>>(p);
-
-    k_route<<<U_,256,0,stream>>>(p);
-    k_xscale<<<U_,256,0,stream>>>(p);
-    k_mgemm<0><<<dim3(9,8,4),256,0,stream>>>(p);
-    k_mhcsel<<<U_,64,0,stream>>>(p);
-    k_he<1><<<2*H_*U_,256,0,stream>>>(p);
-    k_mgemm<1><<<dim3(10,8,48),256,0,stream>>>(p);
-    k_mgemm<2><<<dim3(1,8,48),256,0,stream>>>(p);
-    k_stage2<<<H_*U_,128,0,stream>>>(p);
-    k_stage2q<<<H_*U_,64,0,stream>>>(p);
-    k_mgemm<3><<<dim3(8,8,48),256,0,stream>>>(p);
-    k_scan<<<16,512,0,stream>>>(p);
-    k_mgemm<4><<<dim3(8,8,1),256,0,stream>>>(p);
-    k_final<<<U_,256,0,stream>>>(p);
-  } else {
-    k_tr<<<dim3(32,2,8),256,0,stream>>>(p.W_q, p.WqT, 64, 1024);
-    k_tr<<<dim3(32,2,8),256,0,stream>>>(p.W_k, p.WkT, 64, 1024);
-    k_tr<<<dim3(32,2,8),256,0,stream>>>(p.W_v, p.WvT, 64, 1024);
-    k_tr<<<dim3(16,32,1),256,0,stream>>>(p.W_o, p.WoT, 1024, 512);
-    k_phiT<<<1152,256,0,stream>>>(p);
-    k_route<<<U_,256,0,stream>>>(p);
-    k_xscale<<<U_,256,0,stream>>>(p);
-    k_gemm_f32<0><<<dim3(9,8,4),256,0,stream>>>(p);
-    k_mhcsel<<<U_,64,0,stream>>>(p);
-    k_he<0><<<2*H_*U_,256,0,stream>>>(p);
-    k_gemm_f32<1><<<dim3(10,8,48),256,0,stream>>>(p);
-    k_gemm_f32<2><<<dim3(1,8,48),256,0,stream>>>(p);
-    k_stage2<<<H_*U_,128,0,stream>>>(p);
-    k_stage2q<<<H_*U_,64,0,stream>>>(p);
-    k_gemm_f32<3><<<dim3(8,8,48),256,0,stream>>>(p);
-    k_scan<<<16,512,0,stream>>>(p);
-    k_gemm_f32<4><<<dim3(8,8,1),256,0,stream>>>(p);
-    k_final<<<U_,256,0,stream>>>(p);
-  }
-}
+  hipMemsetAsync(p.pgB, 0, (size_t)H_*U_*320*2, stream);
+  hipMemsetAsync(p.Bt2, 0, (size_t)HE_*128*1024*2, stream);
+
+  k_prep0<<<1152,256,0,stream>>>(p);
+  k_prep1d<<<dim3(150,48),256,0,stream>>>(p);
+  size_t b1s = (size_t)1216*1024;
+  k_prept<<<dim3(32, 4,48),256,0,stream>>>(p.a_up,  (long)1024*DA_, DA_, DA_, p.Bt1+ 128*1024, b1s, 1024, 1024, 1024);
+  k_prept<<<dim3(32, 4,48),256,0,stream>>>(p.b_up,  (long)1024*DA_, DA_, DA_, p.Bt1+ 231*1024, b1s, 1024, 1024, 1024);
+  k_prept<<<dim3(32,16,48),256,0,stream>>>(p.W_pre, (long)1024*CC_, CC_, CC_, p.Bt1+ 334*1024, b1s, 1024, 1024, 1024);
+  k_prept<<<dim3(32,10,48),256,0,stream>>>(p.W_pg1, (long)1024*DPG_,DPG_,DPG_,p.Bt1+ 846*1024, b1s, 1024, 1024, 1024);
+  k_prept<<<dim3(32, 1,48),256,0,stream>>>(p.lA_k,  (long)1024*R_,  R_,  R_,  p.Bt1+1162*1024, b1s, 1024, 1024, 1024);
+  k_prept<<<dim3(32, 1,48),256,0,stream>>>(p.lA_v,  (long)1024*R_,  R_,  R_,  p.Bt1+1178*1024, b1s, 1024, 1024, 1024);
+  k_prep2d<<<dim3(64,48),256,0,stream>>>(p);
+  k_prept<<<dim3(32, 1,48),256,0,stream>>>(p.lA_q,  (long)1024*R_,  R_,  R_,  p.Bt2+  64*1024, (long)128*1024, 1024, 1024, 1024);
+  k_prept<<<dim3(10,32,48),256,0,stream>>>(p.W_pg2, (long)DPG_*1024,1024,1024,p.Bt3,           (long)1024*320,  320,  320,  316);
+  k_prep4<<<1024,256,0,stream>>>(p);
+
+  k_route<<<U_,256,0,stream>>>(p);
+  k_mgemm<0><<<dim3(9,8,4),256,0,stream>>>(p);
+  k_mhcsel<<<U_,64,0,stream>>>(p);
+  k_he<<<2*H_*U_,256,0,stream>>>(p);
+  k_mgemm<1><<<dim3(10,8,48),256,0,stream>>>(p);
+  k_mgemm<2><<<dim3(1,8,48),256,0,stream>>>(p);
+  k_stage2<<<H_*U_,128,0,stream>>>(p);
+  k_mgemm<3><<<dim3(8,8,48),256,0,stream>>>(p);
+  k_scan<<<16,256,0,stream>>>(p);
+  k_mgemm<4><<<dim3(8,8,1),256,0,stream>>>(p);
+  k_final<<<U_,256,0,stream>>>(p);
+}
```

New measurement: 1.622 ms. 5.6% more time.
